# Optimization experiments

Measured on AMD Instinct MI355X. Metric: run time of the kernel, lower is better.

## Reference

```python
import jax, jax.numpy as jnp
import numpy as np
from jax import lax

DIM = 64
DSTATE = 16
EXPAND = 2
DINNER = DIM * EXPAND
DTRANK = (DIM + 15) // 16  # ceil(d_model/16) = 4
B, D, H, W = 1, 24, 24, 24
EPS = 1e-5


def setup_inputs() -> dict:
    key = jax.random.key(0)
    ks = jax.random.split(key, 40)
    def nrm(i, shape, s=0.02):
        return jax.random.normal(ks[i], shape, jnp.float32) * s
    inp = {}
    inp['x'] = jax.random.normal(ks[0], (B, DIM, D, H, W), jnp.float32)
    # three directional view convs + instance-norm affine params
    inp['w1'] = nrm(1, (DIM, DIM, 3, 1, 1)); inp['b1'] = jnp.zeros((DIM,), jnp.float32)
    inp['g1'] = jnp.ones((DIM,), jnp.float32) + nrm(2, (DIM,)); inp['be1'] = nrm(3, (DIM,))
    inp['w2'] = nrm(4, (DIM, DIM, 1, 3, 1)); inp['b2'] = jnp.zeros((DIM,), jnp.float32)
    inp['g2'] = jnp.ones((DIM,), jnp.float32) + nrm(5, (DIM,)); inp['be2'] = nrm(6, (DIM,))
    inp['w3'] = nrm(7, (DIM, DIM, 1, 1, 3)); inp['b3'] = jnp.zeros((DIM,), jnp.float32)
    inp['g3'] = jnp.ones((DIM,), jnp.float32) + nrm(8, (DIM,)); inp['be3'] = nrm(9, (DIM,))
    # MambaUnit layernorm
    inp['ln_w'] = jnp.ones((DIM,), jnp.float32); inp['ln_b'] = jnp.zeros((DIM,), jnp.float32)
    # Mamba params (shared across the three views, as in the source)
    inp['in_proj_w'] = nrm(10, (2 * DINNER, DIM))
    inp['conv_w'] = jnp.ones((DINNER,), jnp.float32) + nrm(11, (DINNER,))  # d_conv=1 depthwise
    inp['conv_b'] = nrm(12, (DINNER,))
    inp['x_proj_w'] = nrm(13, (DTRANK + 2 * DSTATE, DINNER))
    inp['dt_w'] = nrm(14, (DINNER, DTRANK), 0.1)
    inp['dt_b'] = nrm(15, (DINNER,), 0.1)
    inp['A_log'] = jnp.log(jnp.tile(jnp.arange(1, DSTATE + 1, dtype=jnp.float32), (DINNER, 1)))
    inp['D_param'] = jnp.ones((DINNER,), jnp.float32)
    inp['out_proj_w'] = nrm(16, (DIM, DINNER))
    # fusion 1x1x1 conv + instance norm
    inp['wf'] = nrm(17, (DIM, 3 * DIM, 1, 1, 1)); inp['bf'] = jnp.zeros((DIM,), jnp.float32)
    inp['gf'] = jnp.ones((DIM,), jnp.float32) + nrm(18, (DIM,)); inp['bef'] = nrm(19, (DIM,))
    return inp


def silu(x):
    return x * jax.nn.sigmoid(x)


def conv3d(x, w, b, pad):
    out = lax.conv_general_dilated(
        x, w, (1, 1, 1), [(pad[0], pad[0]), (pad[1], pad[1]), (pad[2], pad[2])],
        dimension_numbers=('NCDHW', 'OIDHW', 'NCDHW'))
    return out + b[None, :, None, None, None]


def instance_norm(x, g, b):
    m = x.mean(axis=(2, 3, 4), keepdims=True)
    v = x.var(axis=(2, 3, 4), keepdims=True)  # biased, as in torch InstanceNorm
    return (x - m) / jnp.sqrt(v + EPS) * g[None, :, None, None, None] + b[None, :, None, None, None]


def layer_norm(x, g, b):
    m = x.mean(axis=-1, keepdims=True)
    v = x.var(axis=-1, keepdims=True)
    return (x - m) / jnp.sqrt(v + EPS) * g + b


def mamba(u, in_proj_w, conv_w, conv_b, x_proj_w, dt_w, dt_b, A_log, D_param, out_proj_w):
    # u: (B, L, d_model)
    xz = u @ in_proj_w.T                       # (B, L, 2*DINNER)
    xi, z = jnp.split(xz, 2, axis=-1)
    xi = silu(xi * conv_w + conv_b)            # d_conv=1 depthwise conv == per-channel affine
    xdbl = xi @ x_proj_w.T                     # (B, L, DTRANK + 2*DSTATE)
    dt = xdbl[..., :DTRANK]
    Bm = xdbl[..., DTRANK:DTRANK + DSTATE]
    Cm = xdbl[..., DTRANK + DSTATE:]
    dt = jax.nn.softplus(dt @ dt_w.T + dt_b)   # (B, L, DINNER)
    A = -jnp.exp(A_log)                        # (DINNER, DSTATE)
    dA = jnp.exp(dt[..., None] * A)            # (B, L, DINNER, DSTATE)
    dBx = dt[..., None] * Bm[:, :, None, :] * xi[..., None]
    def comb(c1, c2):
        a1, b1 = c1
        a2, b2 = c2
        return a1 * a2, a2 * b1 + b2
    _, h = lax.associative_scan(comb, (dA, dBx), axis=1)  # h: (B, L, DINNER, DSTATE)
    y = jnp.einsum('blin,bln->bli', h, Cm) + xi * D_param
    y = y * silu(z)
    return y @ out_proj_w.T


def mamba_unit(x5, ln_w, ln_b, mparams):
    Bb, C = x5.shape[:2]
    dims = x5.shape[2:]
    xf = jnp.transpose(x5.reshape(Bb, C, -1), (0, 2, 1))  # (B, L, C)
    xn = layer_norm(xf, ln_w, ln_b)
    y = mamba(xn, *mparams)
    return jnp.transpose(y, (0, 2, 1)).reshape(Bb, C, *dims)


def reference(x, w1, b1, g1, be1, w2, b2, g2, be2, w3, b3, g3, be3, ln_w, ln_b,
              in_proj_w, conv_w, conv_b, x_proj_w, dt_w, dt_b, A_log, D_param, out_proj_w,
              wf, bf, gf, bef):
    mparams = (in_proj_w, conv_w, conv_b, x_proj_w, dt_w, dt_b, A_log, D_param, out_proj_w)
    v1 = jax.nn.relu(instance_norm(conv3d(x, w1, b1, (1, 0, 0)), g1, be1))
    v2 = jax.nn.relu(instance_norm(conv3d(x, w2, b2, (0, 1, 0)), g2, be2))
    v3 = jax.nn.relu(instance_norm(conv3d(x, w3, b3, (0, 0, 1)), g3, be3))
    m1 = mamba_unit(v1, ln_w, ln_b, mparams)
    m2 = mamba_unit(v2, ln_w, ln_b, mparams)
    m3 = mamba_unit(v3, ln_w, ln_b, mparams)
    cat = jnp.concatenate([m1, m2, m3], axis=1)
    out = jax.nn.relu(instance_norm(conv3d(cat, wf, bf, (0, 0, 0)), gf, bef))
    return out
```

## Files before the change

kernel.cpp:

```cpp
#include <hip/hip_runtime.h>

#define LTOT 13824
#define NCH 108
#define CHL 128
#define EPSF 1e-5f

static const size_t OFF_U   = 1024;
static const size_t NU      = (size_t)3*LTOT*64;
static const size_t NXI     = (size_t)3*LTOT*128;
static const size_t NBM     = (size_t)3*LTOT*16;
static const size_t NAG     = (size_t)3*NCH*128*16;
static const size_t OFF_XIT = OFF_U   + NU;
static const size_t OFF_SZT = OFF_XIT + NXI;
static const size_t OFF_DTT = OFF_SZT + NXI;
static const size_t OFF_BMT = OFF_DTT + NXI;
static const size_t OFF_CMT = OFF_BMT + NBM;
static const size_t OFF_W2  = OFF_CMT + NBM;
static const size_t OFF_WT  = OFF_W2 + 24576;
static const size_t OFF_WI  = OFF_WT + 36864;
static const size_t OFF_AGA = OFF_U;
static const size_t OFF_AGB = OFF_U + NAG;
static const size_t OFF_SEED= OFF_U + 2*NAG;
static const size_t OFF_FIN = OFF_DTT;

__device__ __forceinline__ float sigm(float x){ return 1.f/(1.f+__expf(-x)); }
__device__ __forceinline__ float siluf(float x){ return x*sigm(x); }
__device__ __forceinline__ float softplusf(float x){
    return fmaxf(x,0.f) + log1pf(__expf(-fabsf(x)));
}

template<int CTRL>
__device__ __forceinline__ float dpp_add(float x){
    int v = __builtin_amdgcn_update_dpp(0, __float_as_int(x), CTRL, 0xf, 0xf, true);
    return x + __int_as_float(v);
}
__device__ __forceinline__ float sum16(float x){
    x = dpp_add<0xB1>(x);
    x = dpp_add<0x4E>(x);
    x = dpp_add<0x141>(x);
    x = dpp_add<0x140>(x);
    return x;
}

__global__ __launch_bounds__(256) void k_prep(const float* __restrict__ w1,
                      const float* __restrict__ w2, const float* __restrict__ w3,
                      const float* __restrict__ opw, const float* __restrict__ wf,
                      const float* __restrict__ ipw,
                      float* __restrict__ wt, float* __restrict__ w2t,
                      float* __restrict__ wi)
{
    if (blockIdx.x < 144){
        int idx = blockIdx.x*256 + threadIdx.x;
        int r = idx / 12288, rem = idx % 12288;
        int k = rem >> 6, o = rem & 63;
        const float* W = (r==0)?w1:(r==1)?w2:w3;
        wt[idx] = W[o*192 + k];
    } else if (blockIdx.x < 240){
        int idx = (blockIdx.x-144)*256 + threadIdx.x;
        int o = idx & 63, ri = idx >> 6;
        int r = ri >> 7, i = ri & 127;
        float acc = 0.f;
        for (int c2=0;c2<64;c2++)
            acc += opw[c2*128+i] * wf[o*192 + r*64 + c2];
        w2t[idx] = acc;
    } else {
        int idx = (blockIdx.x-240)*256 + threadIdx.x;
        int col = idx & 255, q = idx >> 8;
        wi[q*256 + col] = ipw[col*64 + q];
    }
}

__global__ __launch_bounds__(192) void k_conv(const float* __restrict__ x,
                       const float* __restrict__ wt,
                       const float* __restrict__ b1, const float* __restrict__ b2,
                       const float* __restrict__ b3,
                       float* __restrict__ u, float* __restrict__ ws)
{
    __shared__ __align__(16) float xs[2*1152];
    __shared__ __align__(16) float wl[48*64];
    __shared__ float ssum[64], ssq[64];
    const int r = blockIdx.y;
    const int row0 = blockIdx.x*2;
    const float* Bz = (r==0)?b1:(r==1)?b2:b3;
    const int tid = threadIdx.x;

    if (tid < 64){ ssum[tid]=0.f; ssq[tid]=0.f; }

    const int rw = (tid >= 96) ? 1 : 0, t2 = tid - rw*96;
    const int og = t2 & 15, wg2 = t2 >> 4;
    const int o0 = og*4, w0 = wg2*4;
    float acc[4][4];
    {
        float b0 = Bz[o0], b1v = Bz[o0+1], b2v = Bz[o0+2], b3v = Bz[o0+3];
        #pragma unroll
        for (int wj=0;wj<4;wj++){ acc[0][wj]=b0; acc[1][wj]=b1v; acc[2][wj]=b2v; acc[3][wj]=b3v; }
    }

    const float* wtr = wt + (size_t)r*12288;
    const float* xrow = &xs[rw*1152];
    const int d0 = (row0)/24,   h0 = (row0)%24;
    const int d1 = (row0+1)/24, h1 = (row0+1)%24;

    for (int ph=0; ph<4; ph++){
        __syncthreads();
        for (int s = tid; s < 3072; s += 192)
            wl[s] = wtr[ph*3072 + s];
        for (int rw2=0; rw2<2; rw2++){
            int row = row0 + rw2;
            int d = rw2 ? d1 : d0, h = rw2 ? h1 : h0;
            for (int s = tid; s < 1152; s += 192){
                int w = s % 24; int kt = s / 24; int ic2 = kt/3, t = kt%3;
                int ic = ph*16 + ic2;
                int src = 0; bool valid = true;
                if (r==0){ int dd = d+t-1; valid = (dd>=0 && dd<24); src = (dd*24+h)*24 + w; }
                else if (r==1){ int hh = h+t-1; valid = (hh>=0 && hh<24); src = (d*24+hh)*24 + w; }
                else { int ww = w+t-1; valid = (ww>=0 && ww<24); src = row*24 + ww; }
                xs[rw2*1152 + s] = valid ? x[(size_t)ic*LTOT + src] : 0.f;
            }
        }
        __syncthreads();
        for (int ic2=0; ic2<16; ic2++){
            #pragma unroll
            for (int t=0;t<3;t++){
                float4 wv = *(const float4*)&wl[(ic2*3+t)*64 + o0];
                float4 xv = *(const float4*)&xrow[(ic2*3+t)*24 + w0];
                acc[0][0]=fmaf(wv.x,xv.x,acc[0][0]); acc[0][1]=fmaf(wv.x,xv.y,acc[0][1]);
                acc[0][2]=fmaf(wv.x,xv.z,acc[0][2]); acc[0][3]=fmaf(wv.x,xv.w,acc[0][3]);
                acc[1][0]=fmaf(wv.y,xv.x,acc[1][0]); acc[1][1]=fmaf(wv.y,xv.y,acc[1][1]);
                acc[1][2]=fmaf(wv.y,xv.z,acc[1][2]); acc[1][3]=fmaf(wv.y,xv.w,acc[1][3]);
                acc[2][0]=fmaf(wv.z,xv.x,acc[2][0]); acc[2][1]=fmaf(wv.z,xv.y,acc[2][1]);
                acc[2][2]=fmaf(wv.z,xv.z,acc[2][2]); acc[2][3]=fmaf(wv.z,xv.w,acc[2][3]);
                acc[3][0]=fmaf(wv.w,xv.x,acc[3][0]); acc[3][1]=fmaf(wv.w,xv.y,acc[3][1]);
                acc[3][2]=fmaf(wv.w,xv.z,acc[3][2]); acc[3][3]=fmaf(wv.w,xv.w,acc[3][3]);
            }
        }
    }

    size_t ub = ((size_t)r*LTOT + (size_t)(row0+rw)*24)*64;
    float ps[4]={0,0,0,0}, pq[4]={0,0,0,0};
    #pragma unroll
    for (int wj=0; wj<4; wj++){
        float4 v = make_float4(acc[0][wj],acc[1][wj],acc[2][wj],acc[3][wj]);
        *(float4*)&u[ub + (size_t)(w0+wj)*64 + o0] = v;
        ps[0]+=v.x; pq[0]+=v.x*v.x; ps[1]+=v.y; pq[1]+=v.y*v.y;
        ps[2]+=v.z; pq[2]+=v.z*v.z; ps[3]+=v.w; pq[3]+=v.w*v.w;
    }
    #pragma unroll
    for (int oj=0;oj<4;oj++){
        atomicAdd(&ssum[o0+oj], ps[oj]);
        atomicAdd(&ssq[o0+oj], pq[oj]);
    }
    __syncthreads();
    if (tid < 64){
        atomicAdd(&ws[r*64 + tid], ssum[tid]);
        atomicAdd(&ws[192 + r*64 + tid], ssq[tid]);
    }
}

__global__ __launch_bounds__(192) void k_stats1(float* ws){
    int t = threadIdx.x;
    float s = ws[t], q = ws[192+t];
    float m = s*(1.f/(float)LTOT);
    float v = q*(1.f/(float)LTOT) - m*m;
    ws[512+t] = m; ws[704+t] = rsqrtf(v + EPSF);
}

__global__ __launch_bounds__(256, 4) void k_inproj(const float* __restrict__ u, float* __restrict__ xiT,
                         float* __restrict__ szT, const float* __restrict__ wi,
                         const float* __restrict__ cw, const float* __restrict__ cb,
                         const float* __restrict__ ws,
                         const float* g1,const float* be1,const float* g2,const float* be2,
                         const float* g3,const float* be3,
                         const float* lnw,const float* lnb)
{
    __shared__ float xl[64*65];
    const int tid = threadIdx.x, r = blockIdx.y;
    const int lane = tid & 63;
    const int wv = __builtin_amdgcn_readfirstlane(tid >> 6);
    const int l0 = blockIdx.x*64;
    size_t gbase = (size_t)r*LTOT + l0;

    {
        const float* g  = (r==0)?g1:(r==1)?g2:g3;
        const float* be = (r==0)?be1:(r==1)?be2:be3;
        float m  = ws[512 + r*64 + lane], rs = ws[704 + r*64 + lane];
        float gg = g[lane], bb = be[lane];
        float lw = lnw[lane], lb = lnb[lane];
        for (int j=0;j<16;j++){
            int p = wv*16 + j;
            float vv = u[(gbase+p)*64 + lane];
            vv = fmaxf((vv-m)*rs*gg + bb, 0.f);
            float s1 = sum16(vv), s2 = sum16(vv*vv);
            s1 += __shfl_xor(s1,16); s2 += __shfl_xor(s2,16);
            s1 += __shfl_xor(s1,32); s2 += __shfl_xor(s2,32);
            float mean = s1*(1.f/64.f);
            float var  = s2*(1.f/64.f) - mean*mean;
            xl[lane*65 + p] = (vv-mean)*rsqrtf(var+EPSF)*lw + lb;
        }
    }
    __syncthreads();

    float acc[64];
    #pragma unroll
    for (int j=0;j<64;j++) acc[j] = 0.f;
    const float* wbase = wi + wv*64;
    for (int q=0;q<64;q++){
        float xq = xl[q*65 + lane];
        const float* wq = wbase + q*256;
        #pragma unroll
        for (int j=0;j<64;j++)
            acc[j] = fmaf(wq[j], xq, acc[j]);
    }

    const bool isx = (wv < 2);
    float* dst = isx ? xiT : szT;
    const int c0 = (wv & 1)*64;
    #pragma unroll
    for (int j=0;j<64;j++){
        int c2 = c0 + j;
        float v;
        if (isx) v = siluf(fmaf(acc[j], cw[c2], cb[c2]));
        else     v = siluf(acc[j]);
        dst[((size_t)r*128 + c2)*LTOT + l0 + lane] = v;
    }
}

__global__ __launch_bounds__(256) void k_xproj(const float* __restrict__ xiT, float* __restrict__ dtT,
                        float* __restrict__ BmT, float* __restrict__ CmT,
                        const float* __restrict__ xpw, const float* __restrict__ dtw,
                        const float* __restrict__ dtb)
{
    __shared__ __align__(16) float xt[128*36];
    __shared__ float ww[36*129];
    __shared__ float sd[4*36];
    const int tid = threadIdx.x, r = blockIdx.y;
    const int l0 = blockIdx.x*32;

    for (int s = tid; s < 4096; s += 256){
        int c = s>>5, p = s&31;
        xt[c*36+p] = xiT[((size_t)r*128 + c)*LTOT + l0 + p];
    }
    for (int s = tid; s < 4608; s += 256){
        int k = s>>7, c = s&127;
        ww[k*129+c] = xpw[s];
    }
    __syncthreads();

    const int wv = tid>>6, lane = tid&63;
    float acc[8] = {0,0,0,0,0,0,0,0};
    if (lane < 36){
        const float* wrow = &ww[lane*129];
        for (int c=0;c<128;c++){
            float w = wrow[c];
            float4 a = *(const float4*)&xt[c*36 + wv*8];
            float4 b = *(const float4*)&xt[c*36 + wv*8 + 4];
            acc[0]=fmaf(w,a.x,acc[0]); acc[1]=fmaf(w,a.y,acc[1]);
            acc[2]=fmaf(w,a.z,acc[2]); acc[3]=fmaf(w,a.w,acc[3]);
            acc[4]=fmaf(w,b.x,acc[4]); acc[5]=fmaf(w,b.y,acc[5]);
            acc[6]=fmaf(w,b.z,acc[6]); acc[7]=fmaf(w,b.w,acc[7]);
        }
    }
    if (lane>=4 && lane<36){
        float* dst = (lane<20) ? BmT : CmT;
        int n = (lane<20) ? (lane-4) : (lane-20);
        size_t base = ((size_t)r*16 + n)*LTOT + l0 + wv*8;
        *(float4*)&dst[base]   = make_float4(acc[0],acc[1],acc[2],acc[3]);
        *(float4*)&dst[base+4] = make_float4(acc[4],acc[5],acc[6],acc[7]);
    }
    if (lane < 4){
        #pragma unroll
        for (int p=0;p<8;p++) sd[lane*36 + wv*8 + p] = acc[p];
    }
    __syncthreads();

    const int i = tid>>1, ph = tid&1;
    float4 dw = *(const float4*)&dtw[i*4];
    float db = dtb[i];
    float buf[16];
    #pragma unroll
    for (int t=0;t<16;t++){
        int p = ph*16 + t;
        float v = db + dw.x*sd[0*36+p] + dw.y*sd[1*36+p]
                     + dw.z*sd[2*36+p] + dw.w*sd[3*36+p];
        buf[t] = softplusf(v);
    }
    size_t base = ((size_t)r*128 + i)*LTOT + l0 + ph*16;
    #pragma unroll
    for (int q=0;q<4;q++){
        *(float4*)&dtT[base + 4*q] =
            make_float4(buf[4*q], buf[4*q+1], buf[4*q+2], buf[4*q+3]);
    }
}

__global__ __launch_bounds__(256) void k_scan1(const float* __restrict__ dtT, const float* __restrict__ BmT,
                        const float* __restrict__ xiT, const float* __restrict__ Alog,
                        float* __restrict__ aga, float* __restrict__ agb)
{
    __shared__ float4 sdt[16*33], sxi[16*33], sbm[16*33];
    const int tid = threadIdx.x;
    const int n = tid & 15, il = tid >> 4;
    const int c = blockIdx.x, ib = blockIdx.y, r = blockIdx.z;
    const int i = ib*16 + il;

    for (int f = tid; f < 512; f += 256){
        int ii = f >> 5, t4 = f & 31;
        size_t rowI = ((size_t)r*128 + ib*16 + ii)*LTOT + (size_t)c*CHL + t4*4;
        size_t rowN = ((size_t)r*16  + ii)*LTOT + (size_t)c*CHL + t4*4;
        sdt[ii*33 + t4] = *(const float4*)&dtT[rowI];
        sxi[ii*33 + t4] = *(const float4*)&xiT[rowI];
        sbm[ii*33 + t4] = *(const float4*)&BmT[rowN];
    }
    __syncthreads();

    const float A2 = -expf(Alog[i*16+n]) * 1.44269504f;
    float b = 0.f, sdtacc = 0.f;
    #define S1_STEP(dv,xv,bv) { float e=exp2f(A2*(dv)); b=fmaf(e,b,(dv)*(xv)*(bv)); }
    for (int t4 = 0; t4 < 32; t4++){
        float4 d = sdt[il*33 + t4];
        float4 x = sxi[il*33 + t4];
        float4 m = sbm[n*33 + t4];
        sdtacc += ((d.x+d.y)+(d.z+d.w));
        S1_STEP(d.x,x.x,m.x) S1_STEP(d.y,x.y,m.y)
        S1_STEP(d.z,x.z,m.z) S1_STEP(d.w,x.w,m.w)
    }
    size_t o = ((size_t)(r*NCH+c)*128 + i)*16 + n;
    aga[o] = exp2f(A2*sdtacc);
    agb[o] = b;
}

__global__ __launch_bounds__(512) void k_scan2(const float* __restrict__ aga, const float* __restrict__ agb,
                        float* __restrict__ seed)
{
    int t = blockIdx.x*512 + threadIdx.x;
    int r = t >> 11, rem = t & 2047;
    float h = 0.f;
    for (int c=0;c<NCH;c++){
        size_t idx = (size_t)(r*NCH+c)*2048 + rem;
        float a = aga[idx], b = agb[idx];
        seed[idx] = h;
        h = fmaf(a, h, b);
    }
}

__global__ __launch_bounds__(256) void k_scan3(const float* __restrict__ dtT, const float* __restrict__ BmT,
                        const float* __restrict__ CmT, const float* __restrict__ xiT,
                        float* __restrict__ szT, const float* __restrict__ Alog,
                        const float* __restrict__ Dp, const float* __restrict__ seed)
{
    __shared__ float4 sdt[16*33], sxi[16*33], sbm[16*33], scm[16*33];
    const int tid = threadIdx.x;
    const int n = tid & 15, il = tid >> 4;
    const int c = blockIdx.x, ib = blockIdx.y, r = blockIdx.z;
    const int i = ib*16 + il;

    for (int f = tid; f < 512; f += 256){
        int ii = f >> 5, t4 = f & 31;
        size_t rowI = ((size_t)r*128 + ib*16 + ii)*LTOT + (size_t)c*CHL + t4*4;
        size_t rowN = ((size_t)r*16  + ii)*LTOT + (size_t)c*CHL + t4*4;
        sdt[ii*33 + t4] = *(const float4*)&dtT[rowI];
        sxi[ii*33 + t4] = *(const float4*)&xiT[rowI];
        sbm[ii*33 + t4] = *(const float4*)&BmT[rowN];
        scm[ii*33 + t4] = *(const float4*)&CmT[rowN];
    }
    __syncthreads();

    const float A2 = -expf(Alog[i*16+n]) * 1.44269504f;
    const float Dv = Dp[i];
    float h = seed[(size_t)(r*NCH+c)*2048 + (i*16+n)];

    #define S3_STEP(dv,xv,bv,cv,oyv) { \
        float e=exp2f(A2*(dv)); h=fmaf(e,h,(dv)*(xv)*(bv)); \
        float py=sum16(h*(cv)); oyv = fmaf((xv),Dv,py); }
    for (int t4 = 0; t4 < 32; t4++){
        float4 d = sdt[il*33 + t4];
        float4 x = sxi[il*33 + t4];
        float4 m = sbm[n*33 + t4];
        float4 cv = scm[n*33 + t4];
        float4 yv;
        S3_STEP(d.x,x.x,m.x,cv.x, yv.x)
        S3_STEP(d.y,x.y,m.y,cv.y, yv.y)
        S3_STEP(d.z,x.z,m.z,cv.z, yv.z)
        S3_STEP(d.w,x.w,m.w,cv.w, yv.w)
        if (n==0) sdt[il*33 + t4] = yv;
    }
    __syncthreads();

    for (int f = tid; f < 512; f += 256){
        int ii = f >> 5, t4 = f & 31;
        size_t rowI = ((size_t)r*128 + ib*16 + ii)*LTOT + (size_t)c*CHL + t4*4;
        float4 yv = sdt[ii*33 + t4];
        float4 s  = *(const float4*)&szT[rowI];
        *(float4*)&szT[rowI] = make_float4(yv.x*s.x, yv.y*s.y, yv.z*s.z, yv.w*s.w);
    }
}

__global__ __launch_bounds__(256, 1) void k_fin(const float* __restrict__ yT, const float* __restrict__ w2t,
                      const float* __restrict__ bfb, float* __restrict__ fin,
                      float* __restrict__ ws)
{
    __shared__ __align__(16) float yl[384*20];
    __shared__ float part[4*16*64];
    __shared__ float ssum[64], ssq[64];
    const int tid = threadIdx.x;
    const int l0 = blockIdx.x*16;
    const int o = tid & 63, sg = tid >> 6;

    for (int f = tid; f < 6144; f += 256){
        int k = f >> 4, p = f & 15;
        yl[k*20 + p] = yT[(size_t)k*LTOT + l0 + p];
    }
    float wreg[96];
    {
        const float* wp = w2t + (size_t)(sg*96)*64 + o;
        #pragma unroll
        for (int j=0;j<96;j++) wreg[j] = wp[(size_t)j*64];
    }
    if (tid < 64){ ssum[tid]=0.f; ssq[tid]=0.f; }
    __syncthreads();

    float acc[16];
    #pragma unroll
    for (int p=0;p<16;p++) acc[p]=0.f;
    const float* ylbase = &yl[sg*96*20];
    #pragma unroll
    for (int j=0;j<96;j++){
        float w = wreg[j];
        const float4* yp4 = (const float4*)&ylbase[j*20];
        float4 a = yp4[0], b = yp4[1], c = yp4[2], d = yp4[3];
        acc[0] =fmaf(w,a.x,acc[0]);  acc[1] =fmaf(w,a.y,acc[1]);
        acc[2] =fmaf(w,a.z,acc[2]);  acc[3] =fmaf(w,a.w,acc[3]);
        acc[4] =fmaf(w,b.x,acc[4]);  acc[5] =fmaf(w,b.y,acc[5]);
        acc[6] =fmaf(w,b.z,acc[6]);  acc[7] =fmaf(w,b.w,acc[7]);
        acc[8] =fmaf(w,c.x,acc[8]);  acc[9] =fmaf(w,c.y,acc[9]);
        acc[10]=fmaf(w,c.z,acc[10]); acc[11]=fmaf(w,c.w,acc[11]);
        acc[12]=fmaf(w,d.x,acc[12]); acc[13]=fmaf(w,d.y,acc[13]);
        acc[14]=fmaf(w,d.z,acc[14]); acc[15]=fmaf(w,d.w,acc[15]);
    }
    #pragma unroll
    for (int p=0;p<16;p++) part[(sg*16+p)*64 + o] = acc[p];
    __syncthreads();

    float bias = bfb[o];
    float ps=0.f, pq=0.f;
    #pragma unroll
    for (int j=0;j<4;j++){
        int p = sg + j*4;
        float s = part[(0*16+p)*64+o] + part[(1*16+p)*64+o]
                + part[(2*16+p)*64+o] + part[(3*16+p)*64+o] + bias;
        fin[(size_t)(l0+p)*64 + o] = s;
        ps += s; pq += s*s;
    }
    atomicAdd(&ssum[o], ps); atomicAdd(&ssq[o], pq);
    __syncthreads();
    if (tid<64){
        atomicAdd(&ws[384+tid], ssum[tid]);
        atomicAdd(&ws[448+tid], ssq[tid]);
    }
}

__global__ __launch_bounds__(64) void k_statsF(float* ws){
    int t = threadIdx.x;
    float s = ws[384+t], q = ws[448+t];
    float m = s*(1.f/(float)LTOT);
    float v = q*(1.f/(float)LTOT) - m*m;
    ws[896+t] = m; ws[960+t] = rsqrtf(v + EPSF);
}

__global__ __launch_bounds__(256) void k_out(const float* __restrict__ fin, const float* __restrict__ ws,
                      const float* __restrict__ gf, const float* __restrict__ bef,
                      float* __restrict__ out)
{
    __shared__ float tl[64*65];
    const int tid = threadIdx.x;
    const int l0 = blockIdx.x*64;
    for (int s=tid; s<4096; s+=256){
        int li = s>>6, o = s&63;
        float v = fin[(size_t)(l0+li)*64 + o];
        v = fmaxf((v - ws[896+o])*ws[960+o]*gf[o] + bef[o], 0.f);
        tl[o*65+li] = v;
    }
    __syncthreads();
    for (int s=tid; s<4096; s+=256){
        int o = s>>6, li = s&63;
        out[(size_t)o*LTOT + l0 + li] = tl[o*65+li];
    }
}

extern "C" void kernel_launch(void* const* d_in, const int* in_sizes, int n_in,
                              void* d_out, int out_size, void* d_ws, size_t ws_size,
                              hipStream_t stream)
{
    const float* X    = (const float*)d_in[0];
    const float* W1   = (const float*)d_in[1];  const float* B1  = (const float*)d_in[2];
    const float* G1   = (const float*)d_in[3];  const float* BE1 = (const float*)d_in[4];
    const float* W2   = (const float*)d_in[5];  const float* B2  = (const float*)d_in[6];
    const float* G2   = (const float*)d_in[7];  const float* BE2 = (const float*)d_in[8];
    const float* W3   = (const float*)d_in[9];  const float* B3  = (const float*)d_in[10];
    const float* G3   = (const float*)d_in[11]; const float* BE3 = (const float*)d_in[12];
    const float* LNW  = (const float*)d_in[13]; const float* LNB = (const float*)d_in[14];
    const float* IPW  = (const float*)d_in[15];
    const float* CW   = (const float*)d_in[16]; const float* CB  = (const float*)d_in[17];
    const float* XPW  = (const float*)d_in[18];
    const float* DTW  = (const float*)d_in[19]; const float* DTB = (const float*)d_in[20];
    const float* ALOG = (const float*)d_in[21]; const float* DP  = (const float*)d_in[22];
    const float* OPW  = (const float*)d_in[23];
    const float* WF   = (const float*)d_in[24]; const float* BF  = (const float*)d_in[25];
    const float* GF   = (const float*)d_in[26]; const float* BEF = (const float*)d_in[27];
    float* ws = (float*)d_ws;

    (void)hipMemsetAsync(d_ws, 0, 2048, stream);

    k_prep  <<<304, 256, 0, stream>>>(W1, W2, W3, OPW, WF, IPW,
                                      ws+OFF_WT, ws+OFF_W2, ws+OFF_WI);
    k_conv  <<<dim3(288,3), 192, 0, stream>>>(X, ws+OFF_WT, B1, B2, B3, ws+OFF_U, ws);
    k_stats1<<<1, 192, 0, stream>>>(ws);
    k_inproj<<<dim3(216,3), 256, 0, stream>>>(ws+OFF_U, ws+OFF_XIT, ws+OFF_SZT,
                                              ws+OFF_WI, CW, CB, ws,
                                              G1,BE1,G2,BE2,G3,BE3, LNW,LNB);
    k_xproj <<<dim3(432,3), 256, 0, stream>>>(ws+OFF_XIT, ws+OFF_DTT, ws+OFF_BMT,
                                              ws+OFF_CMT, XPW, DTW, DTB);
    k_scan1 <<<dim3(NCH,8,3), 256, 0, stream>>>(ws+OFF_DTT, ws+OFF_BMT, ws+OFF_XIT,
                                                ALOG, ws+OFF_AGA, ws+OFF_AGB);
    k_scan2 <<<12, 512, 0, stream>>>(ws+OFF_AGA, ws+OFF_AGB, ws+OFF_SEED);
    k_scan3 <<<dim3(NCH,8,3), 256, 0, stream>>>(ws+OFF_DTT, ws+OFF_BMT, ws+OFF_CMT,
                                                ws+OFF_XIT, ws+OFF_SZT, ALOG, DP,
                                                ws+OFF_SEED);
    k_fin   <<<864, 256, 0, stream>>>(ws+OFF_SZT, ws+OFF_W2, BF, ws+OFF_FIN, ws);
    k_statsF<<<1, 64, 0, stream>>>(ws);
    k_out   <<<216, 256, 0, stream>>>(ws+OFF_FIN, ws, GF, BEF, (float*)d_out);
}
```

Baseline: 374.3 us.

## Switch intermediates to position-major layout and register-tile scan over states

Intermediate tensors xi, sz, dt, B and C move from channel-major (channel, position) to position-major (position, channel) storage. Producers and consumers (in-proj, x-proj, scans, final conv) are rewritten to match. The scan kernels drop shared-memory staging and use 64-thread blocks where each thread holds 4 states in registers, reading global memory directly and reducing the C-projection with DPP adds across 4 lanes. This is meant to cut shared-memory traffic and the 16-lane reduction, at the cost of strided scalar global loads and lower per-block parallelism in the scans.

```diff
diff --git a/kernel.cpp b/kernel.cpp
--- a/kernel.cpp
+++ b/kernel.cpp
@@ -215,13 +215,20 @@
     const bool isx = (wv < 2);
     float* dst = isx ? xiT : szT;
     const int c0 = (wv & 1)*64;
-    #pragma unroll
-    for (int j=0;j<64;j++){
-        int c2 = c0 + j;
-        float v;
-        if (isx) v = siluf(fmaf(acc[j], cw[c2], cb[c2]));
-        else     v = siluf(acc[j]);
-        dst[((size_t)r*128 + c2)*LTOT + l0 + lane] = v;
+    float* row = dst + ((size_t)r*LTOT + l0 + lane)*128 + c0;
+    #pragma unroll
+    for (int j=0;j<64;j+=4){
+        float v0,v1,v2,v3;
+        if (isx){
+            v0 = siluf(fmaf(acc[j+0], cw[c0+j+0], cb[c0+j+0]));
+            v1 = siluf(fmaf(acc[j+1], cw[c0+j+1], cb[c0+j+1]));
+            v2 = siluf(fmaf(acc[j+2], cw[c0+j+2], cb[c0+j+2]));
+            v3 = siluf(fmaf(acc[j+3], cw[c0+j+3], cb[c0+j+3]));
+        } else {
+            v0 = siluf(acc[j+0]); v1 = siluf(acc[j+1]);
+            v2 = siluf(acc[j+2]); v3 = siluf(acc[j+3]);
+        }
+        *(float4*)&row[j] = make_float4(v0,v1,v2,v3);
     }
 }
 
@@ -237,8 +244,8 @@
     const int l0 = blockIdx.x*32;
 
     for (int s = tid; s < 4096; s += 256){
-        int c = s>>5, p = s&31;
-        xt[c*36+p] = xiT[((size_t)r*128 + c)*LTOT + l0 + p];
+        int cc = s & 127, p = s >> 7;
+        xt[cc*36 + p] = xiT[((size_t)r*LTOT + l0 + p)*128 + cc];
     }
     for (int s = tid; s < 4608; s += 256){
         int k = s>>7, c = s&127;
@@ -263,9 +270,9 @@
     if (lane>=4 && lane<36){
         float* dst = (lane<20) ? BmT : CmT;
         int n = (lane<20) ? (lane-4) : (lane-20);
-        size_t base = ((size_t)r*16 + n)*LTOT + l0 + wv*8;
-        *(float4*)&dst[base]   = make_float4(acc[0],acc[1],acc[2],acc[3]);
-        *(float4*)&dst[base+4] = make_float4(acc[4],acc[5],acc[6],acc[7]);
+        size_t rowb = (size_t)r*LTOT + l0 + wv*8;
+        #pragma unroll
+        for (int p=0;p<8;p++) dst[(rowb+p)*16 + n] = acc[p];
     }
     if (lane < 4){
         #pragma unroll
@@ -284,48 +291,49 @@
                      + dw.z*sd[2*36+p] + dw.w*sd[3*36+p];
         buf[t] = softplusf(v);
     }
-    size_t base = ((size_t)r*128 + i)*LTOT + l0 + ph*16;
-    #pragma unroll
-    for (int q=0;q<4;q++){
-        *(float4*)&dtT[base + 4*q] =
-            make_float4(buf[4*q], buf[4*q+1], buf[4*q+2], buf[4*q+3]);
-    }
-}
-
-__global__ __launch_bounds__(256) void k_scan1(const float* __restrict__ dtT, const float* __restrict__ BmT,
+    size_t lb = (size_t)r*LTOT + l0 + ph*16;
+    #pragma unroll
+    for (int t=0;t<16;t++) dtT[(lb+t)*128 + i] = buf[t];
+}
+
+__global__ __launch_bounds__(64) void k_scan1(const float* __restrict__ dtT, const float* __restrict__ BmT,
                         const float* __restrict__ xiT, const float* __restrict__ Alog,
                         float* __restrict__ aga, float* __restrict__ agb)
 {
-    __shared__ float4 sdt[16*33], sxi[16*33], sbm[16*33];
     const int tid = threadIdx.x;
-    const int n = tid & 15, il = tid >> 4;
+    const int ng = tid & 3, il = tid >> 2;
     const int c = blockIdx.x, ib = blockIdx.y, r = blockIdx.z;
     const int i = ib*16 + il;
 
-    for (int f = tid; f < 512; f += 256){
-        int ii = f >> 5, t4 = f & 31;
-        size_t rowI = ((size_t)r*128 + ib*16 + ii)*LTOT + (size_t)c*CHL + t4*4;
-        size_t rowN = ((size_t)r*16  + ii)*LTOT + (size_t)c*CHL + t4*4;
-        sdt[ii*33 + t4] = *(const float4*)&dtT[rowI];
-        sxi[ii*33 + t4] = *(const float4*)&xiT[rowI];
-        sbm[ii*33 + t4] = *(const float4*)&BmT[rowN];
-    }
-    __syncthreads();
-
-    const float A2 = -expf(Alog[i*16+n]) * 1.44269504f;
-    float b = 0.f, sdtacc = 0.f;
-    #define S1_STEP(dv,xv,bv) { float e=exp2f(A2*(dv)); b=fmaf(e,b,(dv)*(xv)*(bv)); }
-    for (int t4 = 0; t4 < 32; t4++){
-        float4 d = sdt[il*33 + t4];
-        float4 x = sxi[il*33 + t4];
-        float4 m = sbm[n*33 + t4];
-        sdtacc += ((d.x+d.y)+(d.z+d.w));
-        S1_STEP(d.x,x.x,m.x) S1_STEP(d.y,x.y,m.y)
-        S1_STEP(d.z,x.z,m.z) S1_STEP(d.w,x.w,m.w)
-    }
-    size_t o = ((size_t)(r*NCH+c)*128 + i)*16 + n;
-    aga[o] = exp2f(A2*sdtacc);
-    agb[o] = b;
+    float A2[4];
+    #pragma unroll
+    for (int k=0;k<4;k++) A2[k] = -expf(Alog[i*16 + ng*4 + k]) * 1.44269504f;
+
+    size_t lbase = (size_t)r*LTOT + (size_t)c*CHL;
+    const float* dp = dtT + lbase*128 + i;
+    const float* xp = xiT + lbase*128 + i;
+    const float* bp = BmT + lbase*16 + ng*4;
+
+    float b0=0.f,b1=0.f,b2=0.f,b3=0.f, dsum=0.f;
+    for (int t4=0; t4<CHL/4; t4++){
+        #pragma unroll
+        for (int u2=0;u2<4;u2++){
+            float d  = dp[u2*128];
+            float xv = xp[u2*128];
+            float4 Bv = *(const float4*)&bp[u2*16];
+            float dx = d*xv;
+            dsum += d;
+            b0 = fmaf(exp2f(A2[0]*d), b0, dx*Bv.x);
+            b1 = fmaf(exp2f(A2[1]*d), b1, dx*Bv.y);
+            b2 = fmaf(exp2f(A2[2]*d), b2, dx*Bv.z);
+            b3 = fmaf(exp2f(A2[3]*d), b3, dx*Bv.w);
+        }
+        dp += 512; xp += 512; bp += 64;
+    }
+    size_t o = ((size_t)(r*NCH+c)*128 + i)*16 + ng*4;
+    *(float4*)&aga[o] = make_float4(exp2f(A2[0]*dsum), exp2f(A2[1]*dsum),
+                                    exp2f(A2[2]*dsum), exp2f(A2[3]*dsum));
+    *(float4*)&agb[o] = make_float4(b0,b1,b2,b3);
 }
 
 __global__ __launch_bounds__(512) void k_scan2(const float* __restrict__ aga, const float* __restrict__ agb,
@@ -342,55 +350,51 @@
     }
 }
 
-__global__ __launch_bounds__(256) void k_scan3(const float* __restrict__ dtT, const float* __restrict__ BmT,
+__global__ __launch_bounds__(64) void k_scan3(const float* __restrict__ dtT, const float* __restrict__ BmT,
                         const float* __restrict__ CmT, const float* __restrict__ xiT,
                         float* __restrict__ szT, const float* __restrict__ Alog,
                         const float* __restrict__ Dp, const float* __restrict__ seed)
 {
-    __shared__ float4 sdt[16*33], sxi[16*33], sbm[16*33], scm[16*33];
     const int tid = threadIdx.x;
-    const int n = tid & 15, il = tid >> 4;
+    const int ng = tid & 3, il = tid >> 2;
     const int c = blockIdx.x, ib = blockIdx.y, r = blockIdx.z;
     const int i = ib*16 + il;
 
-    for (int f = tid; f < 512; f += 256){
-        int ii = f >> 5, t4 = f & 31;
-        size_t rowI = ((size_t)r*128 + ib*16 + ii)*LTOT + (size_t)c*CHL + t4*4;
-        size_t rowN = ((size_t)r*16  + ii)*LTOT + (size_t)c*CHL + t4*4;
-        sdt[ii*33 + t4] = *(const float4*)&dtT[rowI];
-        sxi[ii*33 + t4] = *(const float4*)&xiT[rowI];
-        sbm[ii*33 + t4] = *(const float4*)&BmT[rowN];
-        scm[ii*33 + t4] = *(const float4*)&CmT[rowN];
-    }
-    __syncthreads();
-
-    const float A2 = -expf(Alog[i*16+n]) * 1.44269504f;
+    float A2[4];
+    #pragma unroll
+    for (int k=0;k<4;k++) A2[k] = -expf(Alog[i*16 + ng*4 + k]) * 1.44269504f;
     const float Dv = Dp[i];
-    float h = seed[(size_t)(r*NCH+c)*2048 + (i*16+n)];
-
-    #define S3_STEP(dv,xv,bv,cv,oyv) { \
-        float e=exp2f(A2*(dv)); h=fmaf(e,h,(dv)*(xv)*(bv)); \
-        float py=sum16(h*(cv)); oyv = fmaf((xv),Dv,py); }
-    for (int t4 = 0; t4 < 32; t4++){
-        float4 d = sdt[il*33 + t4];
-        float4 x = sxi[il*33 + t4];
-        float4 m = sbm[n*33 + t4];
-        float4 cv = scm[n*33 + t4];
-        float4 yv;
-        S3_STEP(d.x,x.x,m.x,cv.x, yv.x)
-        S3_STEP(d.y,x.y,m.y,cv.y, yv.y)
-        S3_STEP(d.z,x.z,m.z,cv.z, yv.z)
-        S3_STEP(d.w,x.w,m.w,cv.w, yv.w)
-        if (n==0) sdt[il*33 + t4] = yv;
-    }
-    __syncthreads();
-
-    for (int f = tid; f < 512; f += 256){
-        int ii = f >> 5, t4 = f & 31;
-        size_t rowI = ((size_t)r*128 + ib*16 + ii)*LTOT + (size_t)c*CHL + t4*4;
-        float4 yv = sdt[ii*33 + t4];
-        float4 s  = *(const float4*)&szT[rowI];
-        *(float4*)&szT[rowI] = make_float4(yv.x*s.x, yv.y*s.y, yv.z*s.z, yv.w*s.w);
+
+    float4 h4 = *(const float4*)&seed[((size_t)(r*NCH+c)*128 + i)*16 + ng*4];
+    float h0=h4.x, h1=h4.y, h2=h4.z, h3=h4.w;
+
+    size_t lbase = (size_t)r*LTOT + (size_t)c*CHL;
+    const float* dp = dtT + lbase*128 + i;
+    const float* xp = xiT + lbase*128 + i;
+    const float* bp = BmT + lbase*16 + ng*4;
+    const float* cp = CmT + lbase*16 + ng*4;
+    float* sp = szT + lbase*128 + i;
+
+    for (int t4=0; t4<CHL/4; t4++){
+        #pragma unroll
+        for (int u2=0;u2<4;u2++){
+            float d  = dp[u2*128];
+            float xv = xp[u2*128];
+            float4 Bv = *(const float4*)&bp[u2*16];
+            float4 Cv = *(const float4*)&cp[u2*16];
+            float dx = d*xv;
+            h0 = fmaf(exp2f(A2[0]*d), h0, dx*Bv.x);
+            h1 = fmaf(exp2f(A2[1]*d), h1, dx*Bv.y);
+            h2 = fmaf(exp2f(A2[2]*d), h2, dx*Bv.z);
+            h3 = fmaf(exp2f(A2[3]*d), h3, dx*Bv.w);
+            float p = h0*Cv.x + h1*Cv.y + h2*Cv.z + h3*Cv.w;
+            p = dpp_add<0xB1>(p);
+            p = dpp_add<0x4E>(p);
+            float s = sp[u2*128];
+            float out = fmaf(xv, Dv, p) * s;
+            if (ng == 0) sp[u2*128] = out;
+        }
+        dp += 512; xp += 512; bp += 64; cp += 64; sp += 512;
     }
 }
 
@@ -406,8 +410,9 @@
     const int o = tid & 63, sg = tid >> 6;
 
     for (int f = tid; f < 6144; f += 256){
-        int k = f >> 4, p = f & 15;
-        yl[k*20 + p] = yT[(size_t)k*LTOT + l0 + p];
+        int p = f / 384, k = f - p*384;
+        int r2 = k >> 7, c2 = k & 127;
+        yl[k*20 + p] = yT[((size_t)r2*LTOT + l0 + p)*128 + c2];
     }
     float wreg[96];
     {
@@ -519,12 +524,12 @@
                                               G1,BE1,G2,BE2,G3,BE3, LNW,LNB);
     k_xproj <<<dim3(432,3), 256, 0, stream>>>(ws+OFF_XIT, ws+OFF_DTT, ws+OFF_BMT,
                                               ws+OFF_CMT, XPW, DTW, DTB);
-    k_scan1 <<<dim3(NCH,8,3), 256, 0, stream>>>(ws+OFF_DTT, ws+OFF_BMT, ws+OFF_XIT,
-                                                ALOG, ws+OFF_AGA, ws+OFF_AGB);
+    k_scan1 <<<dim3(NCH,8,3), 64, 0, stream>>>(ws+OFF_DTT, ws+OFF_BMT, ws+OFF_XIT,
+                                               ALOG, ws+OFF_AGA, ws+OFF_AGB);
     k_scan2 <<<12, 512, 0, stream>>>(ws+OFF_AGA, ws+OFF_AGB, ws+OFF_SEED);
-    k_scan3 <<<dim3(NCH,8,3), 256, 0, stream>>>(ws+OFF_DTT, ws+OFF_BMT, ws+OFF_CMT,
-                                                ws+OFF_XIT, ws+OFF_SZT, ALOG, DP,
-                                                ws+OFF_SEED);
+    k_scan3 <<<dim3(NCH,8,3), 64, 0, stream>>>(ws+OFF_DTT, ws+OFF_BMT, ws+OFF_CMT,
+                                               ws+OFF_XIT, ws+OFF_SZT, ALOG, DP,
+                                               ws+OFF_SEED);
     k_fin   <<<864, 256, 0, stream>>>(ws+OFF_SZT, ws+OFF_W2, BF, ws+OFF_FIN, ws);
     k_statsF<<<1, 64, 0, stream>>>(ws);
     k_out   <<<216, 256, 0, stream>>>(ws+OFF_FIN, ws, GF, BEF, (float*)d_out);
```

New measurement: 433.0 us. 1.16x slower.

## Scan kernels: each thread owns four states, 64 channels per block

Applied to the files above, without the earlier changes.

The chunked selective-scan kernels are remapped so each thread handles four state indices of one channel instead of one. A block now covers 64 channels in two 64-step halves. This lets the dt*x product and the shared-memory loads of dt/x be reused across four states, and replaces the 16-lane sum16 reduction in scan3 with two DPP adds across 4 lanes. The grid shrinks from 2592 to 648 blocks and per-thread register pressure rises, which may reduce parallelism and occupancy.

```diff
diff --git a/kernel.cpp b/kernel.cpp
--- a/kernel.cpp
+++ b/kernel.cpp
@@ -296,36 +296,62 @@
                         const float* __restrict__ xiT, const float* __restrict__ Alog,
                         float* __restrict__ aga, float* __restrict__ agb)
 {
-    __shared__ float4 sdt[16*33], sxi[16*33], sbm[16*33];
+    __shared__ __align__(16) float sdt[64*68];
+    __shared__ __align__(16) float sxi[64*68];
+    __shared__ __align__(16) float sbm[16*68];
     const int tid = threadIdx.x;
-    const int n = tid & 15, il = tid >> 4;
+    const int ng = tid & 3, il = tid >> 2;
     const int c = blockIdx.x, ib = blockIdx.y, r = blockIdx.z;
-    const int i = ib*16 + il;
-
-    for (int f = tid; f < 512; f += 256){
-        int ii = f >> 5, t4 = f & 31;
-        size_t rowI = ((size_t)r*128 + ib*16 + ii)*LTOT + (size_t)c*CHL + t4*4;
-        size_t rowN = ((size_t)r*16  + ii)*LTOT + (size_t)c*CHL + t4*4;
-        sdt[ii*33 + t4] = *(const float4*)&dtT[rowI];
-        sxi[ii*33 + t4] = *(const float4*)&xiT[rowI];
-        sbm[ii*33 + t4] = *(const float4*)&BmT[rowN];
-    }
-    __syncthreads();
-
-    const float A2 = -expf(Alog[i*16+n]) * 1.44269504f;
-    float b = 0.f, sdtacc = 0.f;
-    #define S1_STEP(dv,xv,bv) { float e=exp2f(A2*(dv)); b=fmaf(e,b,(dv)*(xv)*(bv)); }
-    for (int t4 = 0; t4 < 32; t4++){
-        float4 d = sdt[il*33 + t4];
-        float4 x = sxi[il*33 + t4];
-        float4 m = sbm[n*33 + t4];
-        sdtacc += ((d.x+d.y)+(d.z+d.w));
-        S1_STEP(d.x,x.x,m.x) S1_STEP(d.y,x.y,m.y)
-        S1_STEP(d.z,x.z,m.z) S1_STEP(d.w,x.w,m.w)
-    }
-    size_t o = ((size_t)(r*NCH+c)*128 + i)*16 + n;
-    aga[o] = exp2f(A2*sdtacc);
-    agb[o] = b;
+    const int i = ib*64 + il;
+
+    float A2[4];
+    #pragma unroll
+    for (int k=0;k<4;k++) A2[k] = -expf(Alog[i*16 + ng*4 + k]) * 1.44269504f;
+
+    const size_t rowDX = ((size_t)r*128 + ib*64)*LTOT + (size_t)c*CHL;
+    const size_t rowB  = ((size_t)r*16)*LTOT + (size_t)c*CHL;
+
+    float b0=0.f,b1=0.f,b2=0.f,b3=0.f, dsum=0.f;
+
+    for (int hh=0; hh<2; hh++){
+        __syncthreads();
+        const int lb = hh*64;
+        for (int f = tid; f < 1024; f += 256){
+            int row = f >> 4, t4 = f & 15;
+            *(float4*)&sdt[row*68 + t4*4] = *(const float4*)&dtT[rowDX + (size_t)row*LTOT + lb + t4*4];
+            *(float4*)&sxi[row*68 + t4*4] = *(const float4*)&xiT[rowDX + (size_t)row*LTOT + lb + t4*4];
+        }
+        for (int f = tid; f < 256; f += 256){
+            int row = f >> 4, t4 = f & 15;
+            *(float4*)&sbm[row*68 + t4*4] = *(const float4*)&BmT[rowB + (size_t)row*LTOT + lb + t4*4];
+        }
+        __syncthreads();
+
+        for (int t4 = 0; t4 < 16; t4++){
+            float4 d4 = *(const float4*)&sdt[il*68 + t4*4];
+            float4 x4 = *(const float4*)&sxi[il*68 + t4*4];
+            float4 B0 = *(const float4*)&sbm[(ng*4+0)*68 + t4*4];
+            float4 B1 = *(const float4*)&sbm[(ng*4+1)*68 + t4*4];
+            float4 B2 = *(const float4*)&sbm[(ng*4+2)*68 + t4*4];
+            float4 B3 = *(const float4*)&sbm[(ng*4+3)*68 + t4*4];
+            #define S1Q(dv,xv,c0,c1,c2,c3) { \
+                float dx = (dv)*(xv); dsum += (dv); \
+                b0 = fmaf(exp2f(A2[0]*(dv)), b0, dx*(c0)); \
+                b1 = fmaf(exp2f(A2[1]*(dv)), b1, dx*(c1)); \
+                b2 = fmaf(exp2f(A2[2]*(dv)), b2, dx*(c2)); \
+                b3 = fmaf(exp2f(A2[3]*(dv)), b3, dx*(c3)); }
+            S1Q(d4.x, x4.x, B0.x, B1.x, B2.x, B3.x)
+            S1Q(d4.y, x4.y, B0.y, B1.y, B2.y, B3.y)
+            S1Q(d4.z, x4.z, B0.z, B1.z, B2.z, B3.z)
+            S1Q(d4.w, x4.w, B0.w, B1.w, B2.w, B3.w)
+            #undef S1Q
+        }
+    }
+
+    size_t o = ((size_t)(r*NCH+c)*128 + i)*16 + ng*4;
+    *(float4*)&aga[o] = make_float4(exp2f(A2[0]*dsum), exp2f(A2[1]*dsum),
+                                    exp2f(A2[2]*dsum), exp2f(A2[3]*dsum));
+    *(float4*)&agb[o] = make_float4(b0,b1,b2,b3);
 }
 
 __global__ __launch_bounds__(512) void k_scan2(const float* __restrict__ aga, const float* __restrict__ agb,
@@ -347,50 +373,82 @@
                         float* __restrict__ szT, const float* __restrict__ Alog,
                         const float* __restrict__ Dp, const float* __restrict__ seed)
 {
-    __shared__ float4 sdt[16*33], sxi[16*33], sbm[16*33], scm[16*33];
+    __shared__ __align__(16) float sdt[64*68];
+    __shared__ __align__(16) float sxi[64*68];
+    __shared__ __align__(16) float sbm[16*68];
+    __shared__ __align__(16) float scm[16*68];
     const int tid = threadIdx.x;
-    const int n = tid & 15, il = tid >> 4;
+    const int ng = tid & 3, il = tid >> 2;
     const int c = blockIdx.x, ib = blockIdx.y, r = blockIdx.z;
-    const int i = ib*16 + il;
-
-    for (int f = tid; f < 512; f += 256){
-        int ii = f >> 5, t4 = f & 31;
-        size_t rowI = ((size_t)r*128 + ib*16 + ii)*LTOT + (size_t)c*CHL + t4*4;
-        size_t rowN = ((size_t)r*16  + ii)*LTOT + (size_t)c*CHL + t4*4;
-        sdt[ii*33 + t4] = *(const float4*)&dtT[rowI];
-        sxi[ii*33 + t4] = *(const float4*)&xiT[rowI];
-        sbm[ii*33 + t4] = *(const float4*)&BmT[rowN];
-        scm[ii*33 + t4] = *(const float4*)&CmT[rowN];
-    }
-    __syncthreads();
-
-    const float A2 = -expf(Alog[i*16+n]) * 1.44269504f;
+    const int i = ib*64 + il;
+
+    float A2[4];
+    #pragma unroll
+    for (int k=0;k<4;k++) A2[k] = -expf(Alog[i*16 + ng*4 + k]) * 1.44269504f;
     const float Dv = Dp[i];
-    float h = seed[(size_t)(r*NCH+c)*2048 + (i*16+n)];
-
-    #define S3_STEP(dv,xv,bv,cv,oyv) { \
-        float e=exp2f(A2*(dv)); h=fmaf(e,h,(dv)*(xv)*(bv)); \
-        float py=sum16(h*(cv)); oyv = fmaf((xv),Dv,py); }
-    for (int t4 = 0; t4 < 32; t4++){
-        float4 d = sdt[il*33 + t4];
-        float4 x = sxi[il*33 + t4];
-        float4 m = sbm[n*33 + t4];
-        float4 cv = scm[n*33 + t4];
-        float4 yv;
-        S3_STEP(d.x,x.x,m.x,cv.x, yv.x)
-        S3_STEP(d.y,x.y,m.y,cv.y, yv.y)
-        S3_STEP(d.z,x.z,m.z,cv.z, yv.z)
-        S3_STEP(d.w,x.w,m.w,cv.w, yv.w)
-        if (n==0) sdt[il*33 + t4] = yv;
-    }
-    __syncthreads();
-
-    for (int f = tid; f < 512; f += 256){
-        int ii = f >> 5, t4 = f & 31;
-        size_t rowI = ((size_t)r*128 + ib*16 + ii)*LTOT + (size_t)c*CHL + t4*4;
-        float4 yv = sdt[ii*33 + t4];
-        float4 s  = *(const float4*)&szT[rowI];
-        *(float4*)&szT[rowI] = make_float4(yv.x*s.x, yv.y*s.y, yv.z*s.z, yv.w*s.w);
+
+    float4 h4 = *(const float4*)&seed[((size_t)(r*NCH+c)*128 + i)*16 + ng*4];
+    float h0=h4.x, h1=h4.y, h2=h4.z, h3=h4.w;
+
+    const size_t rowDX = ((size_t)r*128 + ib*64)*LTOT + (size_t)c*CHL;
+    const size_t rowB  = ((size_t)r*16)*LTOT + (size_t)c*CHL;
+
+    for (int hh=0; hh<2; hh++){
+        __syncthreads();
+        const int lb = hh*64;
+        for (int f = tid; f < 1024; f += 256){
+            int row = f >> 4, t4 = f & 15;
+            *(float4*)&sdt[row*68 + t4*4] = *(const float4*)&dtT[rowDX + (size_t)row*LTOT + lb + t4*4];
+            *(float4*)&sxi[row*68 + t4*4] = *(const float4*)&xiT[rowDX + (size_t)row*LTOT + lb + t4*4];
+        }
+        for (int f = tid; f < 512; f += 256){
+            int half = f >> 8, f2 = f & 255;
+            int row = f2 >> 4, t4 = f2 & 15;
+            if (half == 0)
+                *(float4*)&sbm[row*68 + t4*4] = *(const float4*)&BmT[rowB + (size_t)row*LTOT + lb + t4*4];
+            else
+                *(float4*)&scm[row*68 + t4*4] = *(const float4*)&CmT[rowB + (size_t)row*LTOT + lb + t4*4];
+        }
+        __syncthreads();
+
+        for (int t4 = 0; t4 < 16; t4++){
+            float4 d4 = *(const float4*)&sdt[il*68 + t4*4];
+            float4 x4 = *(const float4*)&sxi[il*68 + t4*4];
+            float4 B0 = *(const float4*)&sbm[(ng*4+0)*68 + t4*4];
+            float4 B1 = *(const float4*)&sbm[(ng*4+1)*68 + t4*4];
+            float4 B2 = *(const float4*)&sbm[(ng*4+2)*68 + t4*4];
+            float4 B3 = *(const float4*)&sbm[(ng*4+3)*68 + t4*4];
+            float4 C0 = *(const float4*)&scm[(ng*4+0)*68 + t4*4];
+            float4 C1 = *(const float4*)&scm[(ng*4+1)*68 + t4*4];
+            float4 C2 = *(const float4*)&scm[(ng*4+2)*68 + t4*4];
+            float4 C3 = *(const float4*)&scm[(ng*4+3)*68 + t4*4];
+            float4 y4;
+            #define S3Q(dv,xv,b0c,b1c,b2c,b3c,c0c,c1c,c2c,c3c,oy) { \
+                float dx = (dv)*(xv); \
+                h0 = fmaf(exp2f(A2[0]*(dv)), h0, dx*(b0c)); \
+                h1 = fmaf(exp2f(A2[1]*(dv)), h1, dx*(b1c)); \
+                h2 = fmaf(exp2f(A2[2]*(dv)), h2, dx*(b2c)); \
+                h3 = fmaf(exp2f(A2[3]*(dv)), h3, dx*(b3c)); \
+                float p = h0*(c0c); p = fmaf(h1,(c1c),p); \
+                p = fmaf(h2,(c2c),p); p = fmaf(h3,(c3c),p); \
+                p = dpp_add<0xB1>(p); p = dpp_add<0x4E>(p); \
+                oy = fmaf((xv), Dv, p); }
+            S3Q(d4.x,x4.x, B0.x,B1.x,B2.x,B3.x, C0.x,C1.x,C2.x,C3.x, y4.x)
+            S3Q(d4.y,x4.y, B0.y,B1.y,B2.y,B3.y, C0.y,C1.y,C2.y,C3.y, y4.y)
+            S3Q(d4.z,x4.z, B0.z,B1.z,B2.z,B3.z, C0.z,C1.z,C2.z,C3.z, y4.z)
+            S3Q(d4.w,x4.w, B0.w,B1.w,B2.w,B3.w, C0.w,C1.w,C2.w,C3.w, y4.w)
+            #undef S3Q
+            if (ng == 0) *(float4*)&sdt[il*68 + t4*4] = y4;
+        }
+        __syncthreads();
+
+        for (int f = tid; f < 1024; f += 256){
+            int row = f >> 4, t4 = f & 15;
+            size_t gidx = rowDX + (size_t)row*LTOT + lb + t4*4;
+            float4 yv = *(const float4*)&sdt[row*68 + t4*4];
+            float4 s  = *(const float4*)&szT[gidx];
+            *(float4*)&szT[gidx] = make_float4(yv.x*s.x, yv.y*s.y, yv.z*s.z, yv.w*s.w);
+        }
     }
 }
 
@@ -519,10 +577,10 @@
                                               G1,BE1,G2,BE2,G3,BE3, LNW,LNB);
     k_xproj <<<dim3(432,3), 256, 0, stream>>>(ws+OFF_XIT, ws+OFF_DTT, ws+OFF_BMT,
                                               ws+OFF_CMT, XPW, DTW, DTB);
-    k_scan1 <<<dim3(NCH,8,3), 256, 0, stream>>>(ws+OFF_DTT, ws+OFF_BMT, ws+OFF_XIT,
+    k_scan1 <<<dim3(NCH,2,3), 256, 0, stream>>>(ws+OFF_DTT, ws+OFF_BMT, ws+OFF_XIT,
                                                 ALOG, ws+OFF_AGA, ws+OFF_AGB);
     k_scan2 <<<12, 512, 0, stream>>>(ws+OFF_AGA, ws+OFF_AGB, ws+OFF_SEED);
-    k_scan3 <<<dim3(NCH,8,3), 256, 0, stream>>>(ws+OFF_DTT, ws+OFF_BMT, ws+OFF_CMT,
+    k_scan3 <<<dim3(NCH,2,3), 256, 0, stream>>>(ws+OFF_DTT, ws+OFF_BMT, ws+OFF_CMT,
                                                 ws+OFF_XIT, ws+OFF_SZT, ALOG, DP,
                                                 ws+OFF_SEED);
     k_fin   <<<864, 256, 0, stream>>>(ws+OFF_SZT, ws+OFF_W2, BF, ws+OFF_FIN, ws);
```

Result: no change. 373.8 us (-0.1%).
